# Performance work log

Measured on AMD Instinct MI355X. Metric: run time of the kernel, lower is better.

## Reference

```python
import jax, jax.numpy as jnp
import numpy as np

E = 8        # num_local_experts
D = 1024     # d_model
F = 4096     # d_ff
B = 2        # leading (ep/group) dim
T = E * 2048 # dim 1: E chunks of capacity 2048


def setup_inputs() -> dict:
    key = jax.random.key(0)
    ks = jax.random.split(key, 3)
    x = jax.random.normal(ks[0], (B, T, D), dtype=jnp.float32)
    # per-expert FFN params (same init scale as torch Linear default-ish)
    w1 = jax.random.normal(ks[1], (E, D, F), dtype=jnp.float32) * (1.0 / np.sqrt(D))
    b1 = jnp.zeros((E, F), dtype=jnp.float32)
    w2 = jax.random.normal(ks[2], (E, F, D), dtype=jnp.float32) * (1.0 / np.sqrt(F))
    b2 = jnp.zeros((E, D), dtype=jnp.float32)
    return {"x": x, "w1": w1, "b1": b1, "w2": w2, "b2": b2}


def reference(x, w1, b1, w2, b2):
    # torch: inputs.chunk(E, dim=1) -> per-expert FFN -> cat(dim=1)
    # Equivalent batched grouped-GEMM: reshape dim 1 into [E, C].
    b, t, d = x.shape
    c = t // E                                # capacity per expert
    xr = x.reshape(b, E, c, d)                # [B, E, C, D]
    h = jnp.einsum('becd,edf->becf', xr, w1) + b1[None, :, None, :]
    h = jax.nn.gelu(h, approximate=False)     # torch nn.GELU default (erf)
    out = jnp.einsum('becf,efd->becd', h, w2) + b2[None, :, None, :]
    return out.reshape(b, t, d)               # cat along dim=1
```

## Files before the change

### kernel.cpp

```cpp
#include <hip/hip_runtime.h>
#include <math.h>

typedef __bf16 bf16x8 __attribute__((ext_vector_type(8)));
typedef float f32x4 __attribute__((ext_vector_type(4)));

#define BM 256
#define BN 256
#define BK 64

__device__ __forceinline__ unsigned short f2bf(float f) {
    union { float f; unsigned u; } x; x.f = f;
    unsigned r = x.u + 0x7FFFu + ((x.u >> 16) & 1u);
    return (unsigned short)(r >> 16);
}

__device__ __forceinline__ float fast_gelu(float h) {
    const float z  = __builtin_fabsf(h) * 0.70710678118654752f;
    const float t  = __builtin_amdgcn_rcpf(__builtin_fmaf(0.3275911f, z, 1.0f));
    float p = 1.061405429f;
    p = __builtin_fmaf(p, t, -1.453152027f);
    p = __builtin_fmaf(p, t,  1.421413741f);
    p = __builtin_fmaf(p, t, -0.284496736f);
    p = __builtin_fmaf(p, t,  0.254829592f);
    const float ez = __builtin_amdgcn_exp2f(-z * z * 1.4426950408889634f);
    float erfz = __builtin_fmaf(-p * t, ez, 1.0f);
    erfz = (h < 0.0f) ? -erfz : erfz;
    return 0.5f * h * (1.0f + erfz);
}

#define GLOAD_LDS16(GP, LP)                                                      \
    __builtin_amdgcn_global_load_lds(                                            \
        (const __attribute__((address_space(1))) unsigned int*)(GP),             \
        (__attribute__((address_space(3))) unsigned int*)(LP), 16, 0, 0)


#define STAGE_A(sl, h, kto) do {                                                      \
    GLOAD_LDS16(Ag + (size_t)((h) * 128 + 0) * K + (kto), &As[sl][((h) * 128 + stRow + 0) * BK]); \
    GLOAD_LDS16(Ag + (size_t)((h) * 128 + 8) * K + (kto), &As[sl][((h) * 128 + stRow + 8) * BK]); \
} while (0)

#define STAGE_B(sl, h, kto) do {                                                      \
    GLOAD_LDS16(Bg + (size_t)((h) * 128 + 0) * K + (kto), &Bs[sl][((h) * 128 + stRow + 0) * BK]); \
    GLOAD_LDS16(Bg + (size_t)((h) * 128 + 8) * K + (kto), &Bs[sl][((h) * 128 + stRow + 8) * BK]); \
} while (0)

#define LDA(sl, rh) do {                                                              \
    const unsigned short* _pa = &As[sl][((rh) * 128 + wm * 64 + lr) * BK];            \
    _Pragma("unroll") for (int _i = 0; _i < 4; ++_i) {                                \
        af[_i][0] = *(const bf16x8*)&_pa[_i * 16 * BK + pc0];                         \
        af[_i][1] = *(const bf16x8*)&_pa[_i * 16 * BK + pc1];                         \
    }                                                                                 \
} while (0)

#define LDB(sl, ch) do {                                                              \
    const unsigned short* _pb = &Bs[sl][((ch) * 128 + wn * 32 + lr) * BK];            \
    _Pragma("unroll") for (int _j = 0; _j < 2; ++_j) {                                \
        bfr[_j][0] = *(const bf16x8*)&_pb[_j * 16 * BK + pc0];                        \
        bfr[_j][1] = *(const bf16x8*)&_pb[_j * 16 * BK + pc1];                        \
    }                                                                                 \
} while (0)

#define MM(rh, ch) do {                                                               \
    _Pragma("unroll") for (int _i = 0; _i < 4; ++_i)                                  \
    _Pragma("unroll") for (int _j = 0; _j < 2; ++_j) {                                \
        acc[(rh) * 4 + _i][(ch) * 2 + _j] = __builtin_amdgcn_mfma_f32_16x16x32_bf16(  \
            af[_i][0], bfr[_j][0], acc[(rh) * 4 + _i][(ch) * 2 + _j], 0, 0, 0);       \
        acc[(rh) * 4 + _i][(ch) * 2 + _j] = __builtin_amdgcn_mfma_f32_16x16x32_bf16(  \
            af[_i][1], bfr[_j][1], acc[(rh) * 4 + _i][(ch) * 2 + _j], 0, 0, 0);       \
    }                                                                                 \
} while (0)

#define MIDBAR() do {                                                                 \
    __builtin_amdgcn_s_barrier();                                                     \
    asm volatile("s_waitcnt lgkmcnt(0)" ::: "memory");                                \
    __builtin_amdgcn_sched_barrier(0);                                                \
} while (0)

#define ENDBAR_W() do {                                                               \
    asm volatile("s_waitcnt vmcnt(4)" ::: "memory");                                  \
    __builtin_amdgcn_s_barrier();                                                     \
} while (0)

#define ENDBAR_N() do {                                                               \
    asm volatile("" ::: "memory");                                                    \
    __builtin_amdgcn_s_barrier();                                                     \
} while (0)

template <bool GELU, bool OUT_F32>
__global__ __launch_bounds__(512, 2) void gemm_bt(
    const unsigned short* __restrict__ A,
    const unsigned short* __restrict__ Bt,
    const float* __restrict__ bias,
    void* __restrict__ Cv,
    int N, int K, int groupStart, int eStride, int groupPitch)
{
    __shared__ __attribute__((aligned(16))) unsigned short As[2][BM * BK];
    __shared__ __attribute__((aligned(16))) unsigned short Bs[2][BN * BK];

    const int tid  = threadIdx.x;
    const int lane = tid & 63;
    const int w    = tid >> 6;
    const int wm   = w & 1;
    const int wn   = w >> 1;

    const int rowBase = blockIdx.y * BM;
    const int colBase = blockIdx.x * BN;
    const int e = (groupStart + (int)(blockIdx.y >> 3) * eStride) & 7;

    const int sRow   = w * 16 + (lane >> 3);
    const int sChunk = ((lane & 7) ^ (lane >> 3)) * 8;
    const unsigned short* Ag = A + (size_t)(rowBase + sRow) * K + sChunk;
    const unsigned short* Bg = Bt + (size_t)e * N * K
                              + (size_t)(colBase + sRow) * K + sChunk;
    const int stRow = w * 16;

    const int lr  = lane & 15;
    const int q   = lane >> 4;
    const int pc0 = ((0 + q) ^ (lr & 7)) * 8;
    const int pc1 = ((4 + q) ^ (lr & 7)) * 8;

    f32x4 acc[8][4];
    #pragma unroll
    for (int i = 0; i < 8; ++i)
        #pragma unroll
        for (int j = 0; j < 4; ++j)
            acc[i][j] = (f32x4){0.f, 0.f, 0.f, 0.f};

    bf16x8 af[4][2];
    bf16x8 bfr[2][2];

    const int NT = K / BK;

    STAGE_A(0, 0, 0);
    STAGE_B(0, 0, 0);
    STAGE_B(0, 1, 0);
    STAGE_A(0, 1, 0);
    asm volatile("s_waitcnt vmcnt(4)" ::: "memory");
    __builtin_amdgcn_s_barrier();

    for (int t = 0; t < NT; ++t) {
        const int sl  = t & 1;
        const int ns  = sl ^ 1;
        const int ktn = (t + 1 == NT) ? 0 : (t + 1) * BK;

        LDA(sl, 0); LDB(sl, 0);
        STAGE_A(ns, 0, ktn);
        MIDBAR();
        __builtin_amdgcn_s_setprio(1); MM(0, 0); __builtin_amdgcn_s_setprio(0);
        ENDBAR_W();

        LDB(sl, 1);
        STAGE_B(ns, 0, ktn);
        MIDBAR();
        __builtin_amdgcn_s_setprio(1); MM(0, 1); __builtin_amdgcn_s_setprio(0);
        ENDBAR_W();

        LDA(sl, 1);
        STAGE_B(ns, 1, ktn);
        MIDBAR();
        __builtin_amdgcn_s_setprio(1); MM(1, 1); __builtin_amdgcn_s_setprio(0);
        ENDBAR_N();

        LDB(sl, 0);
        STAGE_A(ns, 1, ktn);
        MIDBAR();
        __builtin_amdgcn_s_setprio(1); MM(1, 0); __builtin_amdgcn_s_setprio(0);
        ENDBAR_W();
    }
    asm volatile("s_waitcnt vmcnt(0)" ::: "memory");

    const float* be = bias + (size_t)e * N;
    float bj[2][2];
    #pragma unroll
    for (int ch = 0; ch < 2; ++ch)
        #pragma unroll
        for (int j = 0; j < 2; ++j)
            bj[ch][j] = be[colBase + ch * 128 + wn * 32 + j * 16 + lr];

    #pragma unroll
    for (int rh = 0; rh < 2; ++rh)
    #pragma unroll
    for (int i = 0; i < 4; ++i)
    #pragma unroll
    for (int r = 0; r < 4; ++r) {
        const int rowLocal = rowBase + rh * 128 + wm * 64 + i * 16 + q * 4 + r;
        const int rowG = (rowLocal >> 11) * groupPitch + (rowLocal & 2047);
        #pragma unroll
        for (int ch = 0; ch < 2; ++ch)
        #pragma unroll
        for (int j = 0; j < 2; ++j) {
            const int col = colBase + ch * 128 + wn * 32 + j * 16 + lr;
            float v = acc[rh * 4 + i][ch * 2 + j][r] + bj[ch][j];
            if (GELU) v = fast_gelu(v);
            if (OUT_F32)
                ((float*)Cv)[(size_t)rowG * N + col] = v;
            else
                ((unsigned short*)Cv)[(size_t)rowG * N + col] = f2bf(v);
        }
    }
}

__global__ __launch_bounds__(256) void transpose_cvt(
    const float* __restrict__ W, unsigned short* __restrict__ Wt,
    int R, int C)
{
    __shared__ unsigned short t64[64][68];
    const int t = threadIdx.x;
    const int r0 = blockIdx.y * 64, c0 = blockIdx.x * 64;
    const float* Wp = W + (size_t)blockIdx.z * R * C;
    unsigned short* Wtp = Wt + (size_t)blockIdx.z * R * C;

    #pragma unroll
    for (int p = 0; p < 4; ++p) {
        const int row = p * 16 + (t >> 4);
        const int c4  = (t & 15) * 4;
        float4 v = *(const float4*)&Wp[(size_t)(r0 + row) * C + c0 + c4];
        t64[row][c4 + 0] = f2bf(v.x);
        t64[row][c4 + 1] = f2bf(v.y);
        t64[row][c4 + 2] = f2bf(v.z);
        t64[row][c4 + 3] = f2bf(v.w);
    }
    __syncthreads();
    #pragma unroll
    for (int p = 0; p < 4; ++p) {
        const int oc = p * 16 + (t >> 4);
        const int r4 = (t & 15) * 4;
        ushort4 o;
        o.x = t64[r4 + 0][oc];
        o.y = t64[r4 + 1][oc];
        o.z = t64[r4 + 2][oc];
        o.w = t64[r4 + 3][oc];
        *(ushort4*)&Wtp[(size_t)(c0 + oc) * R + r0 + r4] = o;
    }
}

__global__ __launch_bounds__(256) void cvt_f32_bf16(
    const float* __restrict__ in, unsigned short* __restrict__ out, long long n)
{
    long long i = ((long long)blockIdx.x * 256 + threadIdx.x) * 4;
    if (i < n) {
        float4 v = *(const float4*)&in[i];
        ushort4 o;
        o.x = f2bf(v.x); o.y = f2bf(v.y); o.z = f2bf(v.z); o.w = f2bf(v.w);
        *(ushort4*)&out[i] = o;
    }
}

extern "C" void kernel_launch(void* const* d_in, const int* in_sizes, int n_in,
                              void* d_out, int out_size, void* d_ws, size_t ws_size,
                              hipStream_t stream) {
    const float* x  = (const float*)d_in[0];
    const float* w1 = (const float*)d_in[1];
    const float* b1 = (const float*)d_in[2];
    const float* w2 = (const float*)d_in[3];
    const float* b2 = (const float*)d_in[4];
    float* out = (float*)d_out;
    unsigned short* ws = (unsigned short*)d_ws;

    const int E = 8, D = 1024, F = 4096, Bdim = 2, Cap = 2048;
    const int T = E * Cap;
    const size_t xbE = (size_t)Bdim * T * D;
    const size_t wE  = (size_t)E * D * F;
    const size_t gE  = (size_t)Cap * F;

    dim3 blk(256);
    dim3 gblk(512);
    const size_t fullBytes = (xbE + 2 * wE + gE) * 2;

    if (ws_size >= fullBytes) {
        unsigned short* xb  = ws;
        unsigned short* w1t = ws + xbE;
        unsigned short* w2t = ws + xbE + wE;
        unsigned short* H   = ws + xbE + 2 * wE;
        int gpc = (int)((ws_size / 2 - (xbE + 2 * wE)) / gE);
        if (gpc > 16) gpc = 16;
        if (gpc < 1)  gpc = 1;

        cvt_f32_bf16<<<(unsigned)((xbE / 4 + 255) / 256), blk, 0, stream>>>(x, xb, (long long)xbE);
        transpose_cvt<<<dim3(F / 64, D / 64, E), blk, 0, stream>>>(w1, w1t, D, F);
        transpose_cvt<<<dim3(D / 64, F / 64, E), blk, 0, stream>>>(w2, w2t, F, D);

        for (int g0 = 0; g0 < Bdim * E; g0 += gpc) {
            const int ng = (g0 + gpc <= Bdim * E) ? gpc : (Bdim * E - g0);
            gemm_bt<true, false><<<dim3(F / BN, ng * 8), gblk, 0, stream>>>(
                xb + (size_t)g0 * Cap * D, w1t, b1, H, F, D, g0, 1, 2048);
            gemm_bt<false, true><<<dim3(D / BN, ng * 8), gblk, 0, stream>>>(
                H, w2t, b2, out + (size_t)g0 * Cap * D, D, F, g0, 1, 2048);
        }
    } else {
        unsigned short* w1t = ws;
        unsigned short* w2t = w1t + (size_t)F * D;
        unsigned short* xb  = w2t + (size_t)D * F;
        unsigned short* H   = xb + 2 * (size_t)Cap * D;

        for (int e = 0; e < E; ++e) {
            transpose_cvt<<<dim3(F / 64, D / 64, 1), blk, 0, stream>>>(
                w1 + (size_t)e * D * F, w1t, D, F);
            transpose_cvt<<<dim3(D / 64, F / 64, 1), blk, 0, stream>>>(
                w2 + (size_t)e * F * D, w2t, F, D);
            for (int b = 0; b < Bdim; ++b)
                cvt_f32_bf16<<<(unsigned)(((size_t)Cap * D / 4 + 255) / 256), blk, 0, stream>>>(
                    x + ((size_t)b * T + (size_t)e * Cap) * D,
                    xb + (size_t)b * Cap * D, (long long)Cap * D);
            gemm_bt<true, false><<<dim3(F / BN, 16), gblk, 0, stream>>>(
                xb, w1t, b1, H, F, D, e, 0, 2048);
            gemm_bt<false, true><<<dim3(D / BN, 16), gblk, 0, stream>>>(
                H, w2t, b2, out + (size_t)e * Cap * D, D, F, e, 0, T);
        }
    }
}
```

Measured before the change: 1.085 ms.

## Deepen prefetch pipeline with two-step unrolled K loop and fewer vmcnt waits

Restructures the main GEMM loop to process two K tiles per iteration with explicit buffer indices. Global-to-LDS staging now runs further ahead: part of tile t+1 is prefetched in the prologue and chunks of t+2 and t+3 are issued mid-iteration. Most end-of-phase vmcnt waits become plain barriers, the remaining waits allow more loads in flight, and the sched_barrier is removed. The goal is to hide global load latency better and cut stalls, at the cost of tighter hazard reasoning about LDS slot reuse and a loop that assumes an even tile count.

```diff
diff --git a/kernel.cpp b/kernel.cpp
--- a/kernel.cpp
+++ b/kernel.cpp
@@ -70,20 +70,20 @@
     }                                                                                 \
 } while (0)
 
-#define MIDBAR() do {                                                                 \
+#define MID() do {                                                                    \
     __builtin_amdgcn_s_barrier();                                                     \
-    asm volatile("s_waitcnt lgkmcnt(0)" ::: "memory");                                \
-    __builtin_amdgcn_sched_barrier(0);                                                \
-} while (0)
-
-#define ENDBAR_W() do {                                                               \
-    asm volatile("s_waitcnt vmcnt(4)" ::: "memory");                                  \
+    asm volatile("s_waitcnt lgkmcnt(0)");                                             \
+} while (0)
+
+#define ENDN() do {                                                                   \
     __builtin_amdgcn_s_barrier();                                                     \
-} while (0)
-
-#define ENDBAR_N() do {                                                               \
     asm volatile("" ::: "memory");                                                    \
+} while (0)
+
+#define ENDW() do {                                                                   \
+    asm volatile("s_waitcnt vmcnt(6)" ::: "memory");                                  \
     __builtin_amdgcn_s_barrier();                                                     \
+    asm volatile("" ::: "memory");                                                    \
 } while (0)
 
 template <bool GELU, bool OUT_F32>
@@ -133,39 +133,70 @@
 
     STAGE_A(0, 0, 0);
     STAGE_B(0, 0, 0);
+    STAGE_A(0, 1, 0);
     STAGE_B(0, 1, 0);
-    STAGE_A(0, 1, 0);
     asm volatile("s_waitcnt vmcnt(4)" ::: "memory");
+    STAGE_A(1, 0, BK);
+    STAGE_B(1, 1, BK);
+    STAGE_A(1, 1, BK);
+    asm volatile("s_waitcnt vmcnt(6)" ::: "memory");
     __builtin_amdgcn_s_barrier();
-
-    for (int t = 0; t < NT; ++t) {
-        const int sl  = t & 1;
-        const int ns  = sl ^ 1;
-        const int ktn = (t + 1 == NT) ? 0 : (t + 1) * BK;
-
-        LDA(sl, 0); LDB(sl, 0);
-        STAGE_A(ns, 0, ktn);
-        MIDBAR();
+    asm volatile("" ::: "memory");
+
+    for (int t = 0; t < NT; t += 2) {
+        const int k1 = (t + 1) * BK;
+        const int ku = (t + 2 < NT) ? (t + 2) * BK : 0;
+        const int kv = (t + 3 < NT) ? (t + 3) * BK : 0;
+
+        LDA(0, 0); LDB(0, 0);
+        STAGE_B(1, 0, k1);
+        asm volatile("s_waitcnt lgkmcnt(8)");
+        MID();
         __builtin_amdgcn_s_setprio(1); MM(0, 0); __builtin_amdgcn_s_setprio(0);
-        ENDBAR_W();
-
-        LDB(sl, 1);
-        STAGE_B(ns, 0, ktn);
-        MIDBAR();
+        ENDN();
+
+        LDB(0, 1);
+        STAGE_A(0, 0, ku);
+        MID();
         __builtin_amdgcn_s_setprio(1); MM(0, 1); __builtin_amdgcn_s_setprio(0);
-        ENDBAR_W();
-
-        LDA(sl, 1);
-        STAGE_B(ns, 1, ktn);
-        MIDBAR();
+        ENDN();
+
+        LDA(0, 1);
+        STAGE_B(0, 1, ku);
+        MID();
         __builtin_amdgcn_s_setprio(1); MM(1, 1); __builtin_amdgcn_s_setprio(0);
-        ENDBAR_N();
-
-        LDB(sl, 0);
-        STAGE_A(ns, 1, ktn);
-        MIDBAR();
+        ENDN();
+
+        LDB(0, 0);
+        STAGE_A(0, 1, ku);
+        MID();
         __builtin_amdgcn_s_setprio(1); MM(1, 0); __builtin_amdgcn_s_setprio(0);
-        ENDBAR_W();
+        ENDW();
+
+        LDA(1, 0); LDB(1, 0);
+        STAGE_B(0, 0, ku);
+        asm volatile("s_waitcnt lgkmcnt(8)");
+        MID();
+        __builtin_amdgcn_s_setprio(1); MM(0, 0); __builtin_amdgcn_s_setprio(0);
+        ENDN();
+
+        LDB(1, 1);
+        STAGE_A(1, 0, kv);
+        MID();
+        __builtin_amdgcn_s_setprio(1); MM(0, 1); __builtin_amdgcn_s_setprio(0);
+        ENDN();
+
+        LDA(1, 1);
+        STAGE_B(1, 1, kv);
+        MID();
+        __builtin_amdgcn_s_setprio(1); MM(1, 1); __builtin_amdgcn_s_setprio(0);
+        ENDN();
+
+        LDB(1, 0);
+        STAGE_A(1, 1, kv);
+        MID();
+        __builtin_amdgcn_s_setprio(1); MM(1, 0); __builtin_amdgcn_s_setprio(0);
+        ENDW();
     }
     asm volatile("s_waitcnt vmcnt(0)" ::: "memory");
 
```

Result: faster. 1.037 ms (-4.4%).
